# Performance work log

Measured on AMD Instinct MI355X. Metric: run time of the kernel, lower is better.

## Reference

```python
import jax, jax.numpy as jnp
import numpy as np

C_IN = 32
C_OUT = 32


def setup_inputs() -> dict:
    key = jax.random.key(0)
    k1, k2, k3 = jax.random.split(key, 3)
    B, N, P_DIM = 32, 4096, 64
    X = jax.random.normal(k1, (B, N, C_IN), dtype=jnp.float32)
    P = jax.random.normal(k2, (B, N, P_DIM), dtype=jnp.float32)
    # glorot-ish scale for the hypernetwork Dense kernel (p_dim -> c_in*c_out)
    scale = (2.0 / (P_DIM + C_IN * C_OUT)) ** 0.5
    Wk = jax.random.normal(k3, (P_DIM, C_IN * C_OUT), dtype=jnp.float32) * scale
    return {"X": X, "P": P, "Wk": Wk}


def reference(X, P, Wk):
    B, N, c_in = X.shape
    # hypernetwork: per-position weight generation  [B,N,p] @ [p, c_in*c_out]
    A = jnp.einsum('bnp,pq->bnq', P, Wk)
    W = A.reshape(B, N, c_in, C_OUT)          # [B,N,c_in,c_out]
    W = jax.nn.relu(W)                        # sigma(W)
    # batched per-position GEMV: y_bno = sum_i X_bni * W_bnio
    out = jnp.einsum('bni,bnio->bno', X, W)   # [B,N,c_out]
    return out
```

## Files before the change

### kernel.cpp

```cpp
#include <hip/hip_runtime.h>

#define CI 32
#define CO 32
#define PD 64
#define QDIM 1024
#define M_TOTAL (32*4096)
#define WG_THREADS 512
#define NBLK 512
#define TILE_M 64
#define NT ((M_TOTAL/TILE_M)/NBLK)

typedef float  f32x4  __attribute__((ext_vector_type(4)));
typedef __bf16 bf16x8 __attribute__((ext_vector_type(8)));
typedef __bf16 bf16x4 __attribute__((ext_vector_type(4)));

#define PL_STRIDE 72
#define XL_STRIDE 72
#define OL_STRIDE 44

__global__ __launch_bounds__(256)
void wk_transpose_kernel(const float* __restrict__ Wk, __bf16* __restrict__ wsT)
{
    __shared__ float tile[64][68];
    const int q0 = blockIdx.x * 64;
    const int t  = threadIdx.x;
#pragma unroll
    for (int rr = 0; rr < 4; ++rr) {
        const int k = (t >> 4) + rr * 16;
        const int cc = (t & 15) * 4;
        f32x4 v = *(const f32x4*)(Wk + (size_t)k * QDIM + q0 + cc);
        tile[k][cc] = v[0]; tile[k][cc+1] = v[1]; tile[k][cc+2] = v[2]; tile[k][cc+3] = v[3];
    }
    __syncthreads();
    const int qq = t >> 2, ks = (t & 3) * 16;
    bf16x8 o0, o1;
#pragma unroll
    for (int j = 0; j < 8; ++j) { o0[j] = (__bf16)tile[ks + j][qq]; o1[j] = (__bf16)tile[ks + 8 + j][qq]; }
    *(bf16x8*)(wsT + (size_t)(q0 + qq) * PD + ks)     = o0;
    *(bf16x8*)(wsT + (size_t)(q0 + qq) * PD + ks + 8) = o1;
}

__global__ __launch_bounds__(WG_THREADS, 4)
void cond_dense_kernel(const float* __restrict__ Xg, const float* __restrict__ Pg,
                       const __bf16* __restrict__ wsT, float* __restrict__ outg)
{
    __shared__ __bf16 Pl[TILE_M * PL_STRIDE];
    __shared__ float  Xl[CI * XL_STRIDE];
    __shared__ float  Ol[TILE_M * OL_STRIDE];

    const int tid = threadIdx.x;
    const int l   = tid & 63;
    const int w   = tid >> 6;
    const int h   = l >> 4;
    const int c   = l & 15;
    const int di  = c >> 2;
    const int dq  = c & 3;

    bf16x8 bfA[4][2], bfB[4][2];
#pragma unroll
    for (int tt = 0; tt < 4; ++tt) {
        const int qA = (4*tt + di) * CO + 4*w + dq;
        const int qB = (4*(tt+4) + di) * CO + 4*w + dq;
#pragma unroll
        for (int s = 0; s < 2; ++s) {
            bfA[tt][s] = *(const bf16x8*)(wsT + (size_t)qA * PD + s*32 + h*8);
            bfB[tt][s] = *(const bf16x8*)(wsT + (size_t)qB * PD + s*32 + h*8);
        }
    }

    const int prow = tid >> 4;
    const int pcol = (tid & 15) * 4;
    const int xrow = tid >> 3;
    const int xcol = (tid & 7) * 4;

    f32x4 pr0, pr1, xr;
    auto load_stage = [&](int tile) {
        const float* Pb = Pg + (size_t)tile * TILE_M * PD;
        const float* Xb = Xg + (size_t)tile * TILE_M * CI;
        pr0 = *(const f32x4*)(Pb + prow * PD + pcol);
        pr1 = *(const f32x4*)(Pb + (prow + 32) * PD + pcol);
        xr  = *(const f32x4*)(Xb + xrow * CI + xcol);
    };
    auto write_lds = [&]() {
        bf16x4 a0, a1;
#pragma unroll
        for (int j = 0; j < 4; ++j) { a0[j] = (__bf16)pr0[j]; a1[j] = (__bf16)pr1[j]; }
        *(bf16x4*)(&Pl[prow * PL_STRIDE + pcol])        = a0;
        *(bf16x4*)(&Pl[(prow + 32) * PL_STRIDE + pcol]) = a1;
#pragma unroll
        for (int j = 0; j < 4; ++j) Xl[(xcol + j) * XL_STRIDE + xrow] = xr[j];
    };

    const int tile0 = blockIdx.x * NT;
    load_stage(tile0);
    write_lds();
    __syncthreads();

    for (int it = 0; it < NT; ++it) {
        const int tile = tile0 + it;
        if (it + 1 < NT) load_stage(tile + 1);

#pragma unroll
        for (int sub = 0; sub < 4; ++sub) {
            const int m0 = sub * 16;
            bf16x8 af0 = *(const bf16x8*)(&Pl[(m0 + c) * PL_STRIDE + h*8]);
            bf16x8 af1 = *(const bf16x8*)(&Pl[(m0 + c) * PL_STRIDE + 32 + h*8]);

            f32x4 part = {};
            {
                f32x4 acc[4] = {};
#pragma unroll
                for (int tt = 0; tt < 4; ++tt) {
                    acc[tt] = __builtin_amdgcn_mfma_f32_16x16x32_bf16(af0, bfA[tt][0], acc[tt], 0, 0, 0);
                    acc[tt] = __builtin_amdgcn_mfma_f32_16x16x32_bf16(af1, bfA[tt][1], acc[tt], 0, 0, 0);
                }
#pragma unroll
                for (int tt = 0; tt < 4; ++tt) {
                    const int i = 4*tt + di;
                    f32x4 xv = *(const f32x4*)(&Xl[i * XL_STRIDE + m0 + h*4]);
#pragma unroll
                    for (int r = 0; r < 4; ++r)
                        part[r] += fmaxf(acc[tt][r], 0.0f) * xv[r];
                }
            }
            {
                f32x4 acc[4] = {};
#pragma unroll
                for (int tt = 0; tt < 4; ++tt) {
                    acc[tt] = __builtin_amdgcn_mfma_f32_16x16x32_bf16(af0, bfB[tt][0], acc[tt], 0, 0, 0);
                    acc[tt] = __builtin_amdgcn_mfma_f32_16x16x32_bf16(af1, bfB[tt][1], acc[tt], 0, 0, 0);
                }
#pragma unroll
                for (int tt = 0; tt < 4; ++tt) {
                    const int i = 4*(tt+4) + di;
                    f32x4 xv = *(const f32x4*)(&Xl[i * XL_STRIDE + m0 + h*4]);
#pragma unroll
                    for (int r = 0; r < 4; ++r)
                        part[r] += fmaxf(acc[tt][r], 0.0f) * xv[r];
                }
            }
            const bool b0 = (di & 1) != 0, b1 = (di & 2) != 0;
            const float lo_k = b0 ? part[1] : part[0];
            const float lo_s = b0 ? part[0] : part[1];
            const float hi_k = b0 ? part[3] : part[2];
            const float hi_s = b0 ? part[2] : part[3];
            const float u = lo_k + __shfl_xor(lo_s, 4);
            const float v = hi_k + __shfl_xor(hi_s, 4);
            const float keep = b1 ? v : u;
            const float send = b1 ? u : v;
            const float res = keep + __shfl_xor(send, 8);
            Ol[(m0 + h*4 + di) * OL_STRIDE + w*4 + dq] = res;
        }

        __syncthreads();

        {
            float* outp = outg + (size_t)tile * TILE_M * CO;
            const int row = tid >> 3, col = (tid & 7) * 4;
            f32x4 o = *(const f32x4*)(&Ol[row * OL_STRIDE + col]);
            *(f32x4*)(outp + tid * 4) = o;
        }

        if (it + 1 < NT) {
            write_lds();
            __syncthreads();
        }
    }
}

extern "C" void kernel_launch(void* const* d_in, const int* in_sizes, int n_in,
                              void* d_out, int out_size, void* d_ws, size_t ws_size,
                              hipStream_t stream)
{
    const float* X  = (const float*)d_in[0];
    const float* P  = (const float*)d_in[1];
    const float* Wk = (const float*)d_in[2];
    float* out = (float*)d_out;
    __bf16* wsT = (__bf16*)d_ws;

    wk_transpose_kernel<<<dim3(QDIM / 64), dim3(256), 0, stream>>>(Wk, wsT);
    cond_dense_kernel<<<dim3(NBLK), dim3(WG_THREADS), 0, stream>>>(X, P, wsT, out);
}
```

Measured before the change: 39.77 us.

## Split output columns across blocks to halve resident weight fragments; swizzle P LDS

Each block now computes only 16 of the 32 output channels for its tiles, and the grid is split into two column halves. This halves the per-thread bf16 weight fragments held in registers and so lowers register pressure, at the cost of every P/X tile being loaded and converted twice across the grid. The P tile in LDS drops its padding and uses an XOR swizzle to avoid bank conflicts. The reduction gains an extra shuffle stage, and half the lanes write results.

```diff
diff --git a/kernel.cpp b/kernel.cpp
--- a/kernel.cpp
+++ b/kernel.cpp
@@ -8,15 +8,15 @@
 #define WG_THREADS 512
 #define NBLK 512
 #define TILE_M 64
-#define NT ((M_TOTAL/TILE_M)/NBLK)
+#define NT 8
 
+typedef float  f32x2  __attribute__((ext_vector_type(2)));
 typedef float  f32x4  __attribute__((ext_vector_type(4)));
+typedef __bf16 bf16x4 __attribute__((ext_vector_type(4)));
 typedef __bf16 bf16x8 __attribute__((ext_vector_type(8)));
-typedef __bf16 bf16x4 __attribute__((ext_vector_type(4)));
 
-#define PL_STRIDE 72
 #define XL_STRIDE 72
-#define OL_STRIDE 44
+#define OL_STRIDE 20
 
 __global__ __launch_bounds__(256)
 void wk_transpose_kernel(const float* __restrict__ Wk, __bf16* __restrict__ wsT)
@@ -44,7 +44,7 @@
 void cond_dense_kernel(const float* __restrict__ Xg, const float* __restrict__ Pg,
                        const __bf16* __restrict__ wsT, float* __restrict__ outg)
 {
-    __shared__ __bf16 Pl[TILE_M * PL_STRIDE];
+    __shared__ __bf16 Pl[TILE_M * PD];
     __shared__ float  Xl[CI * XL_STRIDE];
     __shared__ float  Ol[TILE_M * OL_STRIDE];
 
@@ -53,22 +53,27 @@
     const int w   = tid >> 6;
     const int h   = l >> 4;
     const int c   = l & 15;
-    const int di  = c >> 2;
-    const int dq  = c & 3;
+    const int di  = c >> 1;
+    const int dq  = c & 1;
 
-    bf16x8 bfA[4][2], bfB[4][2];
+    const int col0  = (blockIdx.x >> 8) * 16;
+    const int tbase = (blockIdx.x & 255) * NT;
+
+    bf16x8 bfrag[4][2];
 #pragma unroll
-    for (int tt = 0; tt < 4; ++tt) {
-        const int qA = (4*tt + di) * CO + 4*w + dq;
-        const int qB = (4*(tt+4) + di) * CO + 4*w + dq;
+    for (int t = 0; t < 4; ++t) {
+        const int q = (8*t + di) * CO + col0 + 2*w + dq;
 #pragma unroll
-        for (int s = 0; s < 2; ++s) {
-            bfA[tt][s] = *(const bf16x8*)(wsT + (size_t)qA * PD + s*32 + h*8);
-            bfB[tt][s] = *(const bf16x8*)(wsT + (size_t)qB * PD + s*32 + h*8);
-        }
+        for (int s = 0; s < 2; ++s)
+            bfrag[t][s] = *(const bf16x8*)(wsT + (size_t)q * PD + s*32 + h*8);
     }
+#pragma unroll
+    for (int t = 0; t < 4; ++t)
+        asm volatile("" : "+v"(bfrag[t][0]), "+v"(bfrag[t][1]));
 
     const int prow = tid >> 4;
+    const int pg   = (tid & 15) >> 1;
+    const int ph8  = (tid & 1) * 8;
     const int pcol = (tid & 15) * 4;
     const int xrow = tid >> 3;
     const int xcol = (tid & 7) * 4;
@@ -81,84 +86,71 @@
         pr1 = *(const f32x4*)(Pb + (prow + 32) * PD + pcol);
         xr  = *(const f32x4*)(Xb + xrow * CI + xcol);
     };
+    auto pl_ptr = [&](int row) -> __bf16* {
+        return (__bf16*)((char*)Pl + row * 128 + (((pg ^ (row & 7)) << 4) | ph8));
+    };
     auto write_lds = [&]() {
         bf16x4 a0, a1;
 #pragma unroll
         for (int j = 0; j < 4; ++j) { a0[j] = (__bf16)pr0[j]; a1[j] = (__bf16)pr1[j]; }
-        *(bf16x4*)(&Pl[prow * PL_STRIDE + pcol])        = a0;
-        *(bf16x4*)(&Pl[(prow + 32) * PL_STRIDE + pcol]) = a1;
+        *(bf16x4*)pl_ptr(prow)      = a0;
+        *(bf16x4*)pl_ptr(prow + 32) = a1;
 #pragma unroll
         for (int j = 0; j < 4; ++j) Xl[(xcol + j) * XL_STRIDE + xrow] = xr[j];
     };
 
-    const int tile0 = blockIdx.x * NT;
-    load_stage(tile0);
+    load_stage(tbase);
     write_lds();
     __syncthreads();
 
     for (int it = 0; it < NT; ++it) {
-        const int tile = tile0 + it;
+        const int tile = tbase + it;
         if (it + 1 < NT) load_stage(tile + 1);
 
 #pragma unroll
         for (int sub = 0; sub < 4; ++sub) {
             const int m0 = sub * 16;
-            bf16x8 af0 = *(const bf16x8*)(&Pl[(m0 + c) * PL_STRIDE + h*8]);
-            bf16x8 af1 = *(const bf16x8*)(&Pl[(m0 + c) * PL_STRIDE + 32 + h*8]);
+            const char* prow_b = (const char*)Pl + (m0 + c) * 128;
+            bf16x8 af0 = *(const bf16x8*)(prow_b + (((h    ) ^ (c & 7)) << 4));
+            bf16x8 af1 = *(const bf16x8*)(prow_b + (((h + 4) ^ (c & 7)) << 4));
 
+            f32x4 acc[4] = {};
+#pragma unroll
+            for (int t = 0; t < 4; ++t) {
+                acc[t] = __builtin_amdgcn_mfma_f32_16x16x32_bf16(af0, bfrag[t][0], acc[t], 0, 0, 0);
+                acc[t] = __builtin_amdgcn_mfma_f32_16x16x32_bf16(af1, bfrag[t][1], acc[t], 0, 0, 0);
+            }
             f32x4 part = {};
-            {
-                f32x4 acc[4] = {};
 #pragma unroll
-                for (int tt = 0; tt < 4; ++tt) {
-                    acc[tt] = __builtin_amdgcn_mfma_f32_16x16x32_bf16(af0, bfA[tt][0], acc[tt], 0, 0, 0);
-                    acc[tt] = __builtin_amdgcn_mfma_f32_16x16x32_bf16(af1, bfA[tt][1], acc[tt], 0, 0, 0);
-                }
+            for (int t = 0; t < 4; ++t) {
+                const int i = 8*t + di;
+                f32x4 xv = *(const f32x4*)(&Xl[i * XL_STRIDE + m0 + h*4]);
 #pragma unroll
-                for (int tt = 0; tt < 4; ++tt) {
-                    const int i = 4*tt + di;
-                    f32x4 xv = *(const f32x4*)(&Xl[i * XL_STRIDE + m0 + h*4]);
-#pragma unroll
-                    for (int r = 0; r < 4; ++r)
-                        part[r] += fmaxf(acc[tt][r], 0.0f) * xv[r];
-                }
-            }
-            {
-                f32x4 acc[4] = {};
-#pragma unroll
-                for (int tt = 0; tt < 4; ++tt) {
-                    acc[tt] = __builtin_amdgcn_mfma_f32_16x16x32_bf16(af0, bfB[tt][0], acc[tt], 0, 0, 0);
-                    acc[tt] = __builtin_amdgcn_mfma_f32_16x16x32_bf16(af1, bfB[tt][1], acc[tt], 0, 0, 0);
-                }
-#pragma unroll
-                for (int tt = 0; tt < 4; ++tt) {
-                    const int i = 4*(tt+4) + di;
-                    f32x4 xv = *(const f32x4*)(&Xl[i * XL_STRIDE + m0 + h*4]);
-#pragma unroll
-                    for (int r = 0; r < 4; ++r)
-                        part[r] += fmaxf(acc[tt][r], 0.0f) * xv[r];
-                }
+                for (int r = 0; r < 4; ++r)
+                    part[r] += fmaxf(acc[t][r], 0.0f) * xv[r];
             }
             const bool b0 = (di & 1) != 0, b1 = (di & 2) != 0;
             const float lo_k = b0 ? part[1] : part[0];
             const float lo_s = b0 ? part[0] : part[1];
             const float hi_k = b0 ? part[3] : part[2];
             const float hi_s = b0 ? part[2] : part[3];
-            const float u = lo_k + __shfl_xor(lo_s, 4);
-            const float v = hi_k + __shfl_xor(hi_s, 4);
+            const float u = lo_k + __shfl_xor(lo_s, 2);
+            const float v = hi_k + __shfl_xor(hi_s, 2);
             const float keep = b1 ? v : u;
             const float send = b1 ? u : v;
-            const float res = keep + __shfl_xor(send, 8);
-            Ol[(m0 + h*4 + di) * OL_STRIDE + w*4 + dq] = res;
+            const float hf  = keep + __shfl_xor(send, 4);
+            const float res = hf + __shfl_xor(hf, 8);
+            if ((di & 4) == 0)
+                Ol[(m0 + h*4 + (di & 3)) * OL_STRIDE + 2*w + dq] = res;
         }
 
         __syncthreads();
 
         {
-            float* outp = outg + (size_t)tile * TILE_M * CO;
-            const int row = tid >> 3, col = (tid & 7) * 4;
-            f32x4 o = *(const f32x4*)(&Ol[row * OL_STRIDE + col]);
-            *(f32x4*)(outp + tid * 4) = o;
+            float* outp = outg + (size_t)tile * TILE_M * CO + col0;
+            const int row = tid >> 3, cc = (tid & 7) * 2;
+            f32x2 o = *(const f32x2*)(&Ol[row * OL_STRIDE + cc]);
+            *(f32x2*)(outp + row * CO + cc) = o;
         }
 
         if (it + 1 < NT) {
```

Result: no change. 39.99 us (+0.5%).
